# Optimization experiments

Measured on AMD Instinct MI355X. Metric: run time of the kernel, lower is better.

## Reference

```python
import jax, jax.numpy as jnp
import numpy as np

N_NODES = 100000
N_EDGES = 1600000
IN_F, HID_F, OUT_F = 64, 64, 64


def setup_inputs() -> dict:
    key = jax.random.key(0)
    ks = jax.random.split(key, 9)
    return {
        "x": jax.random.normal(ks[0], (N_NODES, IN_F), dtype=jnp.float32),
        "src": jax.random.randint(ks[1], (N_EDGES,), 0, N_NODES, dtype=jnp.int64),
        "dst": jax.random.randint(ks[2], (N_EDGES,), 0, N_NODES, dtype=jnp.int64),
        "W_self1": jax.random.normal(ks[3], (IN_F, HID_F), dtype=jnp.float32) * (1.0 / np.sqrt(IN_F)),
        "W_neigh1": jax.random.normal(ks[4], (IN_F, HID_F), dtype=jnp.float32) * (1.0 / np.sqrt(IN_F)),
        "b1": jnp.zeros((HID_F,), dtype=jnp.float32),
        "W_self2": jax.random.normal(ks[5], (HID_F, OUT_F), dtype=jnp.float32) * (1.0 / np.sqrt(HID_F)),
        "W_neigh2": jax.random.normal(ks[6], (HID_F, OUT_F), dtype=jnp.float32) * (1.0 / np.sqrt(HID_F)),
        "b2": jnp.zeros((OUT_F,), dtype=jnp.float32),
    }


def reference(x, src, dst, W_self1, W_neigh1, b1, W_self2, W_neigh2, b2):
    N = x.shape[0]
    # in-degree per destination node; zero-in-degree nodes get zero aggregate (DGL semantics)
    deg = jax.ops.segment_sum(jnp.ones(dst.shape, dtype=x.dtype), dst, num_segments=N)
    inv_deg = jnp.where(deg > 0, 1.0 / jnp.maximum(deg, 1.0), 0.0)[:, None]  # [N,1]

    def sage_conv(h, W_s, W_n, b):
        # mean over in-neighbors: gather src feats, segment-sum at dst, normalize
        agg = jax.ops.segment_sum(h[src], dst, num_segments=N) * inv_deg  # [N,F]
        return h @ W_s + agg @ W_n + b

    h = jax.nn.relu(sage_conv(x, W_self1, W_neigh1, b1))
    return sage_conv(h, W_self2, W_neigh2, b2)
```

## Files before the change

### kernel.cpp

```cpp
#include <hip/hip_runtime.h>

#define N_NODES 100000
#define N_EDGES 1600000
#define NBKT 196
#define BKT_SHIFT 9
#define BKT_MASK 511
#define NT_TILES 6250
#define CNT_BLOCKS 256

typedef __attribute__((ext_vector_type(8))) short short8;
typedef __attribute__((ext_vector_type(4))) float float4v;

__device__ __forceinline__ unsigned short f2bf(float f) {
  unsigned u = __float_as_uint(f);
  return (unsigned short)((u + 0x7fffu + ((u >> 16) & 1u)) >> 16);
}
__device__ __forceinline__ float bflo(unsigned d) { return __uint_as_float(d << 16); }
__device__ __forceinline__ float bfhi(unsigned d) { return __uint_as_float(d & 0xffff0000u); }

__device__ __forceinline__ void acc_add(float a[8], uint4 v) {
  a[0] += bflo(v.x); a[1] += bfhi(v.x);
  a[2] += bflo(v.y); a[3] += bfhi(v.y);
  a[4] += bflo(v.z); a[5] += bfhi(v.z);
  a[6] += bflo(v.w); a[7] += bfhi(v.w);
}
__device__ __forceinline__ void acc_fma(float a[8], uint4 v, float m) {
  a[0] = fmaf(m, bflo(v.x), a[0]); a[1] = fmaf(m, bfhi(v.x), a[1]);
  a[2] = fmaf(m, bflo(v.y), a[2]); a[3] = fmaf(m, bfhi(v.y), a[3]);
  a[4] = fmaf(m, bflo(v.z), a[4]); a[5] = fmaf(m, bfhi(v.z), a[5]);
  a[6] = fmaf(m, bflo(v.w), a[6]); a[7] = fmaf(m, bfhi(v.w), a[7]);
}


__global__ void k_prep_count(const float* __restrict__ in, unsigned short* __restrict__ outb,
                             const float* __restrict__ W0, const float* __restrict__ W1,
                             const float* __restrict__ W2, const float* __restrict__ W3,
                             unsigned short* __restrict__ F,
                             const int* __restrict__ dst, int* __restrict__ blkCnt) {
  __shared__ int hist[NBKT];
  const int bid = blockIdx.x;
  if (bid < NT_TILES) {
    int i = bid * 256 + threadIdx.x;
    float4 v = ((const float4*)in)[i];
    unsigned d0 = ((unsigned)f2bf(v.y) << 16) | f2bf(v.x);
    unsigned d1 = ((unsigned)f2bf(v.w) << 16) | f2bf(v.z);
    ((uint2*)outb)[i] = make_uint2(d0, d1);
    return;
  }
  if (bid < NT_TILES + 4) {
    if (threadIdx.x >= 64) return;
    const int wsel = bid - NT_TILES;
    const float* W = (wsel == 0) ? W0 : (wsel == 1) ? W1 : (wsel == 2) ? W2 : W3;
    unsigned short* out = F + wsel * 4096;
    int lane = threadIdx.x;
    int col = lane & 15, kr = lane >> 4;
    #pragma unroll
    for (int kc = 0; kc < 2; kc++)
      #pragma unroll
      for (int nt = 0; nt < 4; nt++) {
        unsigned d[4];
        #pragma unroll
        for (int jj = 0; jj < 4; jj++) {
          float w0 = W[(kc * 32 + kr * 8 + 2 * jj)     * 64 + nt * 16 + col];
          float w1 = W[(kc * 32 + kr * 8 + 2 * jj + 1) * 64 + nt * 16 + col];
          d[jj] = ((unsigned)f2bf(w1) << 16) | f2bf(w0);
        }
        uint4* p = (uint4*)(out + ((kc * 4 + nt) * 64 + lane) * 8);
        *p = make_uint4(d[0], d[1], d[2], d[3]);
      }
    return;
  }
  const int cb = bid - NT_TILES - 4;
  for (int t = threadIdx.x; t < NBKT; t += 256) hist[t] = 0;
  __syncthreads();
  const int chunk = N_EDGES / CNT_BLOCKS;
  const int e0 = cb * chunk;
  const int e1 = e0 + chunk;
  for (int e = e0 + threadIdx.x; e < e1; e += 256)
    atomicAdd(&hist[dst[e] >> BKT_SHIFT], 1);
  __syncthreads();
  for (int t = threadIdx.x; t < NBKT; t += 256)
    blkCnt[t * 256 + cb] = hist[t];
}

__global__ void kA_scan1(int* __restrict__ blkCnt, int* __restrict__ bktTot) {
  const int b = blockIdx.x;
  const int tid = threadIdx.x, lane = tid & 63, w = tid >> 6;
  int v = blkCnt[b * 256 + tid];
  int inc = v;
  #pragma unroll
  for (int d = 1; d < 64; d <<= 1) { int y = __shfl_up(inc, d); if (lane >= d) inc += y; }
  __shared__ int wtot[4];
  if (lane == 63) wtot[w] = inc;
  __syncthreads();
  int base = 0;
  for (int j = 0; j < w; j++) base += wtot[j];
  blkCnt[b * 256 + tid] = base + inc - v;
  if (tid == 255) bktTot[b] = base + inc;
}

__global__ void kA_scatter(const int* __restrict__ src, const int* __restrict__ dst,
                           const int* __restrict__ blkCnt, const int* __restrict__ bktTot,
                           int* __restrict__ binned) {
  __shared__ int bs[NBKT];
  __shared__ int curb[NBKT];
  const int tid = threadIdx.x;
  if (tid < 64) {
    int running = 0;
    for (int base = 0; base < NBKT; base += 64) {
      int i = base + tid;
      int v = (i < NBKT) ? bktTot[i] : 0;
      int inc = v;
      #pragma unroll
      for (int d = 1; d < 64; d <<= 1) { int y = __shfl_up(inc, d); if (tid >= d) inc += y; }
      if (i < NBKT) bs[i] = running + inc - v;
      running += __shfl(inc, 63);
    }
  }
  __syncthreads();
  for (int t = tid; t < NBKT; t += 256)
    curb[t] = bs[t] + blkCnt[t * 256 + blockIdx.x];
  __syncthreads();
  const int chunk = N_EDGES / CNT_BLOCKS;
  const int e0 = blockIdx.x * chunk;
  const int e1 = e0 + chunk;
  for (int e = e0 + tid; e < e1; e += 256) {
    int d = dst[e];
    int s = src[e];
    int b = d >> BKT_SHIFT;
    int p = atomicAdd(&curb[b], 1);
    binned[p] = s | ((d & BKT_MASK) << 17);
  }
}


__global__ void k_sort(const int* __restrict__ binned, const int* __restrict__ bktTot,
                       int* __restrict__ off, int* __restrict__ esrc) {
  const int b = blockIdx.x;
  const int tid = threadIdx.x, lane = tid & 63, w = tid >> 6;
  __shared__ int cnt[512];
  __shared__ int pos[512];
  __shared__ int wtot[8];
  __shared__ int s0sh;
  cnt[tid] = 0;
  if (tid < 64) {
    int sum = 0;
    for (int i = tid; i < b; i += 64) sum += bktTot[i];
    #pragma unroll
    for (int m = 1; m < 64; m <<= 1) sum += __shfl_xor(sum, m);
    if (tid == 0) s0sh = sum;
  }
  __syncthreads();
  const int s0 = s0sh, ne = bktTot[b];
  for (int i = tid; i < ne; i += 512)
    atomicAdd(&cnt[binned[s0 + i] >> 17], 1);
  __syncthreads();
  int c = cnt[tid];
  int inc = c;
  #pragma unroll
  for (int d = 1; d < 64; d <<= 1) { int y = __shfl_up(inc, d); if (lane >= d) inc += y; }
  if (lane == 63) wtot[w] = inc;
  __syncthreads();
  int base = s0;
  for (int j = 0; j < w; j++) base += wtot[j];
  int ex = base + inc - c;
  pos[tid] = ex;
  int n0 = (b << BKT_SHIFT) + tid;
  if (n0 < N_NODES) off[n0] = ex;
  if (b == NBKT - 1 && tid == 0) off[N_NODES] = N_EDGES;
  __syncthreads();
  for (int i = tid; i < ne; i += 512) {
    int pe = binned[s0 + i];
    int p = atomicAdd(&pos[pe >> 17], 1);
    esrc[p] = pe & 0x1FFFF;
  }
}


template <bool RELU, bool OUT_BF>
__global__ void k_fused(const unsigned short* __restrict__ featb,
                        const int* __restrict__ off, const int* __restrict__ esrc,
                        const unsigned short* __restrict__ wfS,
                        const unsigned short* __restrict__ wfN,
                        const float* __restrict__ bias,
                        float* __restrict__ outf, unsigned short* __restrict__ outb) {
  __shared__ unsigned short aggl[4][16 * 64];
  const int tid = threadIdx.x;
  const int lane = tid & 63;
  const int wslot = tid >> 6;
  const int t = (blockIdx.x * blockDim.x + tid) >> 6;
  if (t >= NT_TILES) return;

  unsigned short* lw = &aggl[wslot][0];
  const int n = lane >> 3;
  const int h = lane & 7;

  #pragma unroll
  for (int half = 0; half < 2; ++half) {
    const int row = half * 8 + n;
    const int node = t * 16 + row;
    const int o0 = off[node];
    const int o1 = off[node + 1];
    float a[8];
    #pragma unroll
    for (int q = 0; q < 8; q++) a[q] = 0.f;

    int i = o0;
    for (; i + 4 <= o1; i += 4) {
      int s0 = esrc[i], s1 = esrc[i + 1], s2 = esrc[i + 2], s3 = esrc[i + 3];
      uint4 v0 = *(const uint4*)(featb + s0 * 64 + h * 8);
      uint4 v1 = *(const uint4*)(featb + s1 * 64 + h * 8);
      uint4 v2 = *(const uint4*)(featb + s2 * 64 + h * 8);
      uint4 v3 = *(const uint4*)(featb + s3 * 64 + h * 8);
      acc_add(a, v0); acc_add(a, v1); acc_add(a, v2); acc_add(a, v3);
    }
    if (i < o1) {
      int last = o1 - 1;
      int e1 = min(i + 1, last), e2 = min(i + 2, last);
      float m1 = (i + 1 < o1) ? 1.f : 0.f;
      float m2 = (i + 2 < o1) ? 1.f : 0.f;
      int s0 = esrc[i], s1 = esrc[e1], s2 = esrc[e2];
      uint4 v0 = *(const uint4*)(featb + s0 * 64 + h * 8);
      uint4 v1 = *(const uint4*)(featb + s1 * 64 + h * 8);
      uint4 v2 = *(const uint4*)(featb + s2 * 64 + h * 8);
      acc_add(a, v0); acc_fma(a, v1, m1); acc_fma(a, v2, m2);
    }

    const int dg = o1 - o0;
    const float inv = (dg > 0) ? (1.0f / (float)dg) : 0.f;
    unsigned d0 = ((unsigned)f2bf(a[1] * inv) << 16) | f2bf(a[0] * inv);
    unsigned d1 = ((unsigned)f2bf(a[3] * inv) << 16) | f2bf(a[2] * inv);
    unsigned d2 = ((unsigned)f2bf(a[5] * inv) << 16) | f2bf(a[4] * inv);
    unsigned d3 = ((unsigned)f2bf(a[7] * inv) << 16) | f2bf(a[6] * inv);
    *(uint4*)(lw + row * 64 + ((h ^ (row & 7)) << 3)) = make_uint4(d0, d1, d2, d3);
  }

  __builtin_amdgcn_wave_barrier();
  asm volatile("" ::: "memory");

  const int col = lane & 15, rr = lane >> 4;
  const int m = t * 16 + col;
  short8 as0 = *(const short8*)(featb + m * 64 + rr * 8);
  short8 as1 = *(const short8*)(featb + m * 64 + 32 + rr * 8);
  short8 aa0 = *(const short8*)(lw + col * 64 + ((rr ^ (col & 7)) << 3));
  short8 aa1 = *(const short8*)(lw + col * 64 + (((rr + 4) ^ (col & 7)) << 3));

  #pragma unroll
  for (int nt = 0; nt < 4; nt++) {
    short8 bs0 = *(const short8*)(wfS + ((0 * 4 + nt) * 64 + lane) * 8);
    short8 bs1 = *(const short8*)(wfS + ((1 * 4 + nt) * 64 + lane) * 8);
    short8 bn0 = *(const short8*)(wfN + ((0 * 4 + nt) * 64 + lane) * 8);
    short8 bn1 = *(const short8*)(wfN + ((1 * 4 + nt) * 64 + lane) * 8);
    float bvn = bias[nt * 16 + col];
    float4v cfr = {bvn, bvn, bvn, bvn};
    cfr = __builtin_amdgcn_mfma_f32_16x16x32_bf16(as0, bs0, cfr, 0, 0, 0);
    cfr = __builtin_amdgcn_mfma_f32_16x16x32_bf16(as1, bs1, cfr, 0, 0, 0);
    cfr = __builtin_amdgcn_mfma_f32_16x16x32_bf16(aa0, bn0, cfr, 0, 0, 0);
    cfr = __builtin_amdgcn_mfma_f32_16x16x32_bf16(aa1, bn1, cfr, 0, 0, 0);
    #pragma unroll
    for (int r2 = 0; r2 < 4; r2++) {
      int row = t * 16 + rr * 4 + r2;
      float v = cfr[r2];
      if (RELU) v = fmaxf(v, 0.f);
      if (OUT_BF) outb[row * 64 + nt * 16 + col] = f2bf(v);
      else        outf[row * 64 + nt * 16 + col] = v;
    }
  }
}


extern "C" void kernel_launch(void* const* d_in, const int* in_sizes, int n_in,
                              void* d_out, int out_size, void* d_ws, size_t ws_size,
                              hipStream_t stream) {
  const float* x   = (const float*)d_in[0];
  const int*   src = (const int*)d_in[1];
  const int*   dst = (const int*)d_in[2];
  const float* Ws1 = (const float*)d_in[3];
  const float* Wn1 = (const float*)d_in[4];
  const float* b1  = (const float*)d_in[5];
  const float* Ws2 = (const float*)d_in[6];
  const float* Wn2 = (const float*)d_in[7];
  const float* b2  = (const float*)d_in[8];

  char* ws = (char*)d_ws;
  int*            blkCnt   = (int*)(ws + 0);
  int*            bktTot   = (int*)(ws + 262144);
  unsigned short* wf       = (unsigned short*)(ws + 270336);
  int*            binned   = (int*)(ws + 303104);
  int*            off      = (int*)(ws + 6703104);
  int*            esrc     = (int*)(ws + 7103488);
  unsigned short* xbf      = (unsigned short*)(ws + 13503488);
  unsigned short* hbf      = (unsigned short*)(ws + 26303488);

  k_prep_count<<<NT_TILES + 4 + CNT_BLOCKS, 256, 0, stream>>>(
      x, xbf, Ws1, Wn1, Ws2, Wn2, wf, dst, blkCnt);
  kA_scan1<<<NBKT, 256, 0, stream>>>(blkCnt, bktTot);
  kA_scatter<<<CNT_BLOCKS, 256, 0, stream>>>(src, dst, blkCnt, bktTot, binned);
  k_sort<<<NBKT, 512, 0, stream>>>(binned, bktTot, off, esrc);

  k_fused<true, true><<<1563, 256, 0, stream>>>(xbf, off, esrc, wf + 0 * 4096,
                                                wf + 1 * 4096, b1, nullptr, hbf);
  k_fused<false, false><<<1563, 256, 0, stream>>>(hbf, off, esrc, wf + 2 * 4096,
                                                  wf + 3 * 4096, b2, (float*)d_out, nullptr);
}
```

Baseline: 199.7 us.

## Build CSR via global degree atomics, scan, and atomic scatter

Replaces the two-level bucket sort (block histograms, bucket scan, scatter, per-bucket local sort) with a direct CSR build. Degrees are counted with global atomics, exclusive offsets come from a per-block scan that re-sums the preceding degrees, and each edge's source is placed with a global atomic cursor per destination. This removes an intermediate binned buffer and one pass over the edges. In exchange it adds contention on global atomics, a redundant prefix summation in every scan block, and a nondeterministic within-row edge order.

```diff
diff --git a/kernel.cpp b/kernel.cpp
--- a/kernel.cpp
+++ b/kernel.cpp
@@ -2,11 +2,11 @@
 
 #define N_NODES 100000
 #define N_EDGES 1600000
-#define NBKT 196
-#define BKT_SHIFT 9
-#define BKT_MASK 511
 #define NT_TILES 6250
 #define CNT_BLOCKS 256
+#define CVT_BLOCKS 6250
+#define SCAN_BLOCKS 196
+#define PLACE_BLOCKS 1024
 
 typedef __attribute__((ext_vector_type(8))) short short8;
 typedef __attribute__((ext_vector_type(4))) float float4v;
@@ -36,20 +36,18 @@
                              const float* __restrict__ W0, const float* __restrict__ W1,
                              const float* __restrict__ W2, const float* __restrict__ W3,
                              unsigned short* __restrict__ F,
-                             const int* __restrict__ dst, int* __restrict__ blkCnt) {
-  __shared__ int hist[NBKT];
+                             const int* __restrict__ dst, int* __restrict__ deg) {
   const int bid = blockIdx.x;
-  if (bid < NT_TILES) {
-    int i = bid * 256 + threadIdx.x;
-    float4 v = ((const float4*)in)[i];
-    unsigned d0 = ((unsigned)f2bf(v.y) << 16) | f2bf(v.x);
-    unsigned d1 = ((unsigned)f2bf(v.w) << 16) | f2bf(v.z);
-    ((uint2*)outb)[i] = make_uint2(d0, d1);
+  if (bid < CNT_BLOCKS) {
+    const int e0 = bid * (N_EDGES / CNT_BLOCKS);
+    const int e1 = e0 + (N_EDGES / CNT_BLOCKS);
+    for (int e = e0 + threadIdx.x; e < e1; e += 256)
+      atomicAdd(&deg[dst[e]], 1);
     return;
   }
-  if (bid < NT_TILES + 4) {
+  if (bid < CNT_BLOCKS + 4) {
     if (threadIdx.x >= 64) return;
-    const int wsel = bid - NT_TILES;
+    const int wsel = bid - CNT_BLOCKS;
     const float* W = (wsel == 0) ? W0 : (wsel == 1) ? W1 : (wsel == 2) ? W2 : W3;
     unsigned short* out = F + wsel * 4096;
     int lane = threadIdx.x;
@@ -70,109 +68,53 @@
       }
     return;
   }
-  const int cb = bid - NT_TILES - 4;
-  for (int t = threadIdx.x; t < NBKT; t += 256) hist[t] = 0;
+  int i = (bid - CNT_BLOCKS - 4) * 256 + threadIdx.x;
+  float4 v = ((const float4*)in)[i];
+  unsigned d0 = ((unsigned)f2bf(v.y) << 16) | f2bf(v.x);
+  unsigned d1 = ((unsigned)f2bf(v.w) << 16) | f2bf(v.z);
+  ((uint2*)outb)[i] = make_uint2(d0, d1);
+}
+
+
+__global__ __launch_bounds__(512)
+void k_scan(const int* __restrict__ deg, int* __restrict__ off, int* __restrict__ cur) {
+  const int b = blockIdx.x, tid = threadIdx.x, lane = tid & 63, w = tid >> 6;
+  __shared__ int lds[8];
+  int s = 0;
+  for (int i = tid; i < (b << 9); i += 512) s += deg[i];
+  #pragma unroll
+  for (int m = 1; m < 64; m <<= 1) s += __shfl_xor(s, m);
+  if (lane == 0) lds[w] = s;
   __syncthreads();
-  const int chunk = N_EDGES / CNT_BLOCKS;
-  const int e0 = cb * chunk;
-  const int e1 = e0 + chunk;
-  for (int e = e0 + threadIdx.x; e < e1; e += 256)
-    atomicAdd(&hist[dst[e] >> BKT_SHIFT], 1);
+  int bpre = 0;
+  #pragma unroll
+  for (int j = 0; j < 8; j++) bpre += lds[j];
   __syncthreads();
-  for (int t = threadIdx.x; t < NBKT; t += 256)
-    blkCnt[t * 256 + cb] = hist[t];
-}
-
-__global__ void kA_scan1(int* __restrict__ blkCnt, int* __restrict__ bktTot) {
-  const int b = blockIdx.x;
-  const int tid = threadIdx.x, lane = tid & 63, w = tid >> 6;
-  int v = blkCnt[b * 256 + tid];
-  int inc = v;
+  const int n = (b << 9) + tid;
+  int dv = (n < N_NODES) ? deg[n] : 0;
+  int inc = dv;
   #pragma unroll
   for (int d = 1; d < 64; d <<= 1) { int y = __shfl_up(inc, d); if (lane >= d) inc += y; }
-  __shared__ int wtot[4];
-  if (lane == 63) wtot[w] = inc;
+  if (lane == 63) lds[w] = inc;
   __syncthreads();
-  int base = 0;
-  for (int j = 0; j < w; j++) base += wtot[j];
-  blkCnt[b * 256 + tid] = base + inc - v;
-  if (tid == 255) bktTot[b] = base + inc;
-}
-
-__global__ void kA_scatter(const int* __restrict__ src, const int* __restrict__ dst,
-                           const int* __restrict__ blkCnt, const int* __restrict__ bktTot,
-                           int* __restrict__ binned) {
-  __shared__ int bs[NBKT];
-  __shared__ int curb[NBKT];
-  const int tid = threadIdx.x;
-  if (tid < 64) {
-    int running = 0;
-    for (int base = 0; base < NBKT; base += 64) {
-      int i = base + tid;
-      int v = (i < NBKT) ? bktTot[i] : 0;
-      int inc = v;
-      #pragma unroll
-      for (int d = 1; d < 64; d <<= 1) { int y = __shfl_up(inc, d); if (tid >= d) inc += y; }
-      if (i < NBKT) bs[i] = running + inc - v;
-      running += __shfl(inc, 63);
-    }
-  }
-  __syncthreads();
-  for (int t = tid; t < NBKT; t += 256)
-    curb[t] = bs[t] + blkCnt[t * 256 + blockIdx.x];
-  __syncthreads();
-  const int chunk = N_EDGES / CNT_BLOCKS;
+  int wpre = 0;
+  for (int j = 0; j < w; j++) wpre += lds[j];
+  int ex = bpre + wpre + inc - dv;
+  if (n < N_NODES) { off[n] = ex; cur[n] = ex; }
+  if (n == N_NODES - 1) off[N_NODES] = ex + dv;
+}
+
+
+__global__ void k_place(const int* __restrict__ src, const int* __restrict__ dst,
+                        int* __restrict__ cur, int* __restrict__ esrc) {
+  const int chunk = (N_EDGES + PLACE_BLOCKS - 1) / PLACE_BLOCKS;
   const int e0 = blockIdx.x * chunk;
-  const int e1 = e0 + chunk;
-  for (int e = e0 + tid; e < e1; e += 256) {
+  const int e1 = min(e0 + chunk, N_EDGES);
+  for (int e = e0 + threadIdx.x; e < e1; e += 256) {
     int d = dst[e];
     int s = src[e];
-    int b = d >> BKT_SHIFT;
-    int p = atomicAdd(&curb[b], 1);
-    binned[p] = s | ((d & BKT_MASK) << 17);
-  }
-}
-
-
-__global__ void k_sort(const int* __restrict__ binned, const int* __restrict__ bktTot,
-                       int* __restrict__ off, int* __restrict__ esrc) {
-  const int b = blockIdx.x;
-  const int tid = threadIdx.x, lane = tid & 63, w = tid >> 6;
-  __shared__ int cnt[512];
-  __shared__ int pos[512];
-  __shared__ int wtot[8];
-  __shared__ int s0sh;
-  cnt[tid] = 0;
-  if (tid < 64) {
-    int sum = 0;
-    for (int i = tid; i < b; i += 64) sum += bktTot[i];
-    #pragma unroll
-    for (int m = 1; m < 64; m <<= 1) sum += __shfl_xor(sum, m);
-    if (tid == 0) s0sh = sum;
-  }
-  __syncthreads();
-  const int s0 = s0sh, ne = bktTot[b];
-  for (int i = tid; i < ne; i += 512)
-    atomicAdd(&cnt[binned[s0 + i] >> 17], 1);
-  __syncthreads();
-  int c = cnt[tid];
-  int inc = c;
-  #pragma unroll
-  for (int d = 1; d < 64; d <<= 1) { int y = __shfl_up(inc, d); if (lane >= d) inc += y; }
-  if (lane == 63) wtot[w] = inc;
-  __syncthreads();
-  int base = s0;
-  for (int j = 0; j < w; j++) base += wtot[j];
-  int ex = base + inc - c;
-  pos[tid] = ex;
-  int n0 = (b << BKT_SHIFT) + tid;
-  if (n0 < N_NODES) off[n0] = ex;
-  if (b == NBKT - 1 && tid == 0) off[N_NODES] = N_EDGES;
-  __syncthreads();
-  for (int i = tid; i < ne; i += 512) {
-    int pe = binned[s0 + i];
-    int p = atomicAdd(&pos[pe >> 17], 1);
-    esrc[p] = pe & 0x1FFFF;
+    int p = atomicAdd(&cur[d], 1);
+    esrc[p] = s;
   }
 }
 
@@ -283,20 +225,20 @@
   const float* b2  = (const float*)d_in[8];
 
   char* ws = (char*)d_ws;
-  int*            blkCnt   = (int*)(ws + 0);
-  int*            bktTot   = (int*)(ws + 262144);
-  unsigned short* wf       = (unsigned short*)(ws + 270336);
-  int*            binned   = (int*)(ws + 303104);
-  int*            off      = (int*)(ws + 6703104);
-  int*            esrc     = (int*)(ws + 7103488);
-  unsigned short* xbf      = (unsigned short*)(ws + 13503488);
-  unsigned short* hbf      = (unsigned short*)(ws + 26303488);
-
-  k_prep_count<<<NT_TILES + 4 + CNT_BLOCKS, 256, 0, stream>>>(
-      x, xbf, Ws1, Wn1, Ws2, Wn2, wf, dst, blkCnt);
-  kA_scan1<<<NBKT, 256, 0, stream>>>(blkCnt, bktTot);
-  kA_scatter<<<CNT_BLOCKS, 256, 0, stream>>>(src, dst, blkCnt, bktTot, binned);
-  k_sort<<<NBKT, 512, 0, stream>>>(binned, bktTot, off, esrc);
+  int*            deg  = (int*)(ws + 0);
+  int*            off  = (int*)(ws + 400000);
+  int*            cur  = (int*)(ws + 800064);
+  unsigned short* wf   = (unsigned short*)(ws + 1200064);
+  int*            esrc = (int*)(ws + 1232896);
+  unsigned short* xbf  = (unsigned short*)(ws + 7632896);
+  unsigned short* hbf  = (unsigned short*)(ws + 20432896);
+
+  hipMemsetAsync(deg, 0, N_NODES * sizeof(int), stream);
+
+  k_prep_count<<<CNT_BLOCKS + 4 + CVT_BLOCKS, 256, 0, stream>>>(
+      x, xbf, Ws1, Wn1, Ws2, Wn2, wf, dst, deg);
+  k_scan<<<SCAN_BLOCKS, 512, 0, stream>>>(deg, off, cur);
+  k_place<<<PLACE_BLOCKS, 256, 0, stream>>>(src, dst, cur, esrc);
 
   k_fused<true, true><<<1563, 256, 0, stream>>>(xbf, off, esrc, wf + 0 * 4096,
                                                 wf + 1 * 4096, b1, nullptr, hbf);
```

After: 381.3 us. +90.9%, slower.

## Compute per-node degree with global atomics during counting, simplify bucket sort placement

Applied to the files above, without the earlier changes.

The counting pass now also accumulates each node's in-degree with global atomics, so the per-bucket sort kernel can skip its own shared-memory counting pass over binned edges and scan degrees directly. Bucket start offsets are written once by the scatter kernel instead of being re-summed per block. The count/scatter grid doubles to 512 blocks, and edge counting blocks are placed first in the prep launch. This adds 1.6M global atomics and a memset in exchange for removing one read pass over binned data.

```diff
diff --git a/kernel.cpp b/kernel.cpp
--- a/kernel.cpp
+++ b/kernel.cpp
@@ -5,8 +5,11 @@
 #define NBKT 196
 #define BKT_SHIFT 9
 #define BKT_MASK 511
+#define DL_SHIFT 17
+#define SRC_MASK 0x1FFFF
 #define NT_TILES 6250
-#define CNT_BLOCKS 256
+#define CNT_BLOCKS 512
+#define CVT_BLOCKS 6250
 
 typedef __attribute__((ext_vector_type(8))) short short8;
 typedef __attribute__((ext_vector_type(4))) float float4v;
@@ -36,20 +39,28 @@
                              const float* __restrict__ W0, const float* __restrict__ W1,
                              const float* __restrict__ W2, const float* __restrict__ W3,
                              unsigned short* __restrict__ F,
-                             const int* __restrict__ dst, int* __restrict__ blkCnt) {
+                             const int* __restrict__ dst,
+                             int* __restrict__ blkCnt, int* __restrict__ deg) {
   __shared__ int hist[NBKT];
   const int bid = blockIdx.x;
-  if (bid < NT_TILES) {
-    int i = bid * 256 + threadIdx.x;
-    float4 v = ((const float4*)in)[i];
-    unsigned d0 = ((unsigned)f2bf(v.y) << 16) | f2bf(v.x);
-    unsigned d1 = ((unsigned)f2bf(v.w) << 16) | f2bf(v.z);
-    ((uint2*)outb)[i] = make_uint2(d0, d1);
+  if (bid < CNT_BLOCKS) {
+    for (int t = threadIdx.x; t < NBKT; t += 256) hist[t] = 0;
+    __syncthreads();
+    const int e0 = bid * (N_EDGES / CNT_BLOCKS);
+    const int e1 = e0 + (N_EDGES / CNT_BLOCKS);
+    for (int e = e0 + threadIdx.x; e < e1; e += 256) {
+      int d = dst[e];
+      atomicAdd(&hist[d >> BKT_SHIFT], 1);
+      atomicAdd(&deg[d], 1);
+    }
+    __syncthreads();
+    for (int t = threadIdx.x; t < NBKT; t += 256)
+      blkCnt[t * CNT_BLOCKS + bid] = hist[t];
     return;
   }
-  if (bid < NT_TILES + 4) {
+  if (bid < CNT_BLOCKS + 4) {
     if (threadIdx.x >= 64) return;
-    const int wsel = bid - NT_TILES;
+    const int wsel = bid - CNT_BLOCKS;
     const float* W = (wsel == 0) ? W0 : (wsel == 1) ? W1 : (wsel == 2) ? W2 : W3;
     unsigned short* out = F + wsel * 4096;
     int lane = threadIdx.x;
@@ -70,39 +81,36 @@
       }
     return;
   }
-  const int cb = bid - NT_TILES - 4;
-  for (int t = threadIdx.x; t < NBKT; t += 256) hist[t] = 0;
-  __syncthreads();
-  const int chunk = N_EDGES / CNT_BLOCKS;
-  const int e0 = cb * chunk;
-  const int e1 = e0 + chunk;
-  for (int e = e0 + threadIdx.x; e < e1; e += 256)
-    atomicAdd(&hist[dst[e] >> BKT_SHIFT], 1);
-  __syncthreads();
-  for (int t = threadIdx.x; t < NBKT; t += 256)
-    blkCnt[t * 256 + cb] = hist[t];
-}
-
-__global__ void kA_scan1(int* __restrict__ blkCnt, int* __restrict__ bktTot) {
+  int i = (bid - CNT_BLOCKS - 4) * 256 + threadIdx.x;
+  float4 v = ((const float4*)in)[i];
+  unsigned d0 = ((unsigned)f2bf(v.y) << 16) | f2bf(v.x);
+  unsigned d1 = ((unsigned)f2bf(v.w) << 16) | f2bf(v.z);
+  ((uint2*)outb)[i] = make_uint2(d0, d1);
+}
+
+
+__global__ __launch_bounds__(512)
+void kA_scan1(int* __restrict__ blkCnt, int* __restrict__ bktTot) {
   const int b = blockIdx.x;
   const int tid = threadIdx.x, lane = tid & 63, w = tid >> 6;
-  int v = blkCnt[b * 256 + tid];
+  __shared__ int wtot[8];
+  int v = blkCnt[b * CNT_BLOCKS + tid];
   int inc = v;
   #pragma unroll
   for (int d = 1; d < 64; d <<= 1) { int y = __shfl_up(inc, d); if (lane >= d) inc += y; }
-  __shared__ int wtot[4];
   if (lane == 63) wtot[w] = inc;
   __syncthreads();
   int base = 0;
   for (int j = 0; j < w; j++) base += wtot[j];
-  blkCnt[b * 256 + tid] = base + inc - v;
-  if (tid == 255) bktTot[b] = base + inc;
-}
+  blkCnt[b * CNT_BLOCKS + tid] = base + inc - v;
+  if (tid == CNT_BLOCKS - 1) bktTot[b] = base + inc;
+}
+
 
 __global__ void kA_scatter(const int* __restrict__ src, const int* __restrict__ dst,
                            const int* __restrict__ blkCnt, const int* __restrict__ bktTot,
-                           int* __restrict__ binned) {
-  __shared__ int bs[NBKT];
+                           int* __restrict__ bktStart, int* __restrict__ binned) {
+  __shared__ int ps[NBKT];
   __shared__ int curb[NBKT];
   const int tid = threadIdx.x;
   if (tid < 64) {
@@ -113,66 +121,56 @@
       int inc = v;
       #pragma unroll
       for (int d = 1; d < 64; d <<= 1) { int y = __shfl_up(inc, d); if (tid >= d) inc += y; }
-      if (i < NBKT) bs[i] = running + inc - v;
+      if (i < NBKT) ps[i] = running + inc - v;
       running += __shfl(inc, 63);
     }
   }
   __syncthreads();
   for (int t = tid; t < NBKT; t += 256)
-    curb[t] = bs[t] + blkCnt[t * 256 + blockIdx.x];
-  __syncthreads();
-  const int chunk = N_EDGES / CNT_BLOCKS;
-  const int e0 = blockIdx.x * chunk;
-  const int e1 = e0 + chunk;
+    curb[t] = ps[t] + blkCnt[t * CNT_BLOCKS + blockIdx.x];
+  if (blockIdx.x == 0)
+    for (int t = tid; t < NBKT; t += 256) bktStart[t] = ps[t];
+  __syncthreads();
+  const int e0 = blockIdx.x * (N_EDGES / CNT_BLOCKS);
+  const int e1 = e0 + (N_EDGES / CNT_BLOCKS);
   for (int e = e0 + tid; e < e1; e += 256) {
     int d = dst[e];
     int s = src[e];
     int b = d >> BKT_SHIFT;
     int p = atomicAdd(&curb[b], 1);
-    binned[p] = s | ((d & BKT_MASK) << 17);
-  }
-}
-
-
-__global__ void k_sort(const int* __restrict__ binned, const int* __restrict__ bktTot,
-                       int* __restrict__ off, int* __restrict__ esrc) {
+    binned[p] = s | ((d & BKT_MASK) << DL_SHIFT);
+  }
+}
+
+
+__global__ __launch_bounds__(512)
+void k_place(const int* __restrict__ binned, const int* __restrict__ bktStart,
+             const int* __restrict__ bktTot, const int* __restrict__ deg,
+             int* __restrict__ off, int* __restrict__ esrc) {
   const int b = blockIdx.x;
   const int tid = threadIdx.x, lane = tid & 63, w = tid >> 6;
-  __shared__ int cnt[512];
   __shared__ int pos[512];
   __shared__ int wtot[8];
-  __shared__ int s0sh;
-  cnt[tid] = 0;
-  if (tid < 64) {
-    int sum = 0;
-    for (int i = tid; i < b; i += 64) sum += bktTot[i];
-    #pragma unroll
-    for (int m = 1; m < 64; m <<= 1) sum += __shfl_xor(sum, m);
-    if (tid == 0) s0sh = sum;
-  }
-  __syncthreads();
-  const int s0 = s0sh, ne = bktTot[b];
-  for (int i = tid; i < ne; i += 512)
-    atomicAdd(&cnt[binned[s0 + i] >> 17], 1);
-  __syncthreads();
-  int c = cnt[tid];
-  int inc = c;
+  const int s0 = bktStart[b];
+  const int ne = bktTot[b];
+  const int n = (b << BKT_SHIFT) + tid;
+  int dv = (n < N_NODES) ? deg[n] : 0;
+  int inc = dv;
   #pragma unroll
   for (int d = 1; d < 64; d <<= 1) { int y = __shfl_up(inc, d); if (lane >= d) inc += y; }
   if (lane == 63) wtot[w] = inc;
   __syncthreads();
   int base = s0;
   for (int j = 0; j < w; j++) base += wtot[j];
-  int ex = base + inc - c;
+  int ex = base + inc - dv;
   pos[tid] = ex;
-  int n0 = (b << BKT_SHIFT) + tid;
-  if (n0 < N_NODES) off[n0] = ex;
-  if (b == NBKT - 1 && tid == 0) off[N_NODES] = N_EDGES;
+  if (n < N_NODES) off[n] = ex;
+  if (n == N_NODES - 1) off[N_NODES] = ex + dv;
   __syncthreads();
   for (int i = tid; i < ne; i += 512) {
     int pe = binned[s0 + i];
-    int p = atomicAdd(&pos[pe >> 17], 1);
-    esrc[p] = pe & 0x1FFFF;
+    int p = atomicAdd(&pos[pe >> DL_SHIFT], 1);
+    esrc[p] = pe & SRC_MASK;
   }
 }
 
@@ -283,20 +281,24 @@
   const float* b2  = (const float*)d_in[8];
 
   char* ws = (char*)d_ws;
-  int*            blkCnt   = (int*)(ws + 0);
-  int*            bktTot   = (int*)(ws + 262144);
-  unsigned short* wf       = (unsigned short*)(ws + 270336);
-  int*            binned   = (int*)(ws + 303104);
-  int*            off      = (int*)(ws + 6703104);
-  int*            esrc     = (int*)(ws + 7103488);
-  unsigned short* xbf      = (unsigned short*)(ws + 13503488);
-  unsigned short* hbf      = (unsigned short*)(ws + 26303488);
-
-  k_prep_count<<<NT_TILES + 4 + CNT_BLOCKS, 256, 0, stream>>>(
-      x, xbf, Ws1, Wn1, Ws2, Wn2, wf, dst, blkCnt);
-  kA_scan1<<<NBKT, 256, 0, stream>>>(blkCnt, bktTot);
-  kA_scatter<<<CNT_BLOCKS, 256, 0, stream>>>(src, dst, blkCnt, bktTot, binned);
-  k_sort<<<NBKT, 512, 0, stream>>>(binned, bktTot, off, esrc);
+  int*            deg      = (int*)(ws + 0);
+  int*            blkCnt   = (int*)(ws + 400064);
+  int*            bktTot   = (int*)(ws + 801472);
+  int*            bktStart = (int*)(ws + 802496);
+  unsigned short* wf       = (unsigned short*)(ws + 803520);
+  int*            off      = (int*)(ws + 836288);
+  int*            binned   = (int*)(ws + 1236352);
+  int*            esrc     = (int*)(ws + 7636352);
+  unsigned short* xbf      = (unsigned short*)(ws + 14036352);
+  unsigned short* hbf      = (unsigned short*)(ws + 26836352);
+
+  hipMemsetAsync(deg, 0, N_NODES * sizeof(int), stream);
+
+  k_prep_count<<<CNT_BLOCKS + 4 + CVT_BLOCKS, 256, 0, stream>>>(
+      x, xbf, Ws1, Wn1, Ws2, Wn2, wf, dst, blkCnt, deg);
+  kA_scan1<<<NBKT, 512, 0, stream>>>(blkCnt, bktTot);
+  kA_scatter<<<CNT_BLOCKS, 256, 0, stream>>>(src, dst, blkCnt, bktTot, bktStart, binned);
+  k_place<<<NBKT, 512, 0, stream>>>(binned, bktStart, bktTot, deg, off, esrc);
 
   k_fused<true, true><<<1563, 256, 0, stream>>>(xbf, off, esrc, wf + 0 * 4096,
                                                 wf + 1 * 4096, b1, nullptr, hbf);
```

Measured after the change: 256.5 us. 28.4% more time.
